# Kernel optimization log

Measured on AMD Instinct MI355X. Metric: run time of the kernel, lower is better.

The kernel has to match this reference:

```python
import jax, jax.numpy as jnp
import numpy as np

N_NODES = 50000
N_EDGES = 800000
D = 128
N_LAYERS = 3
EPS = 1e-5  # torch LayerNorm default


def _gcn_conv(x, src, dst, dinv, W, b):
    # PyG GCNConv: h = x @ W; out[i] = sum_{(s->i)} dinv[s]*dinv[i]*h[s] + dinv[i]^2*h[i] + b
    h = x @ W
    norm = dinv[src] * dinv[dst]                      # [E]
    msgs = h[src] * norm[:, None]                     # [E, D] gather
    agg = jax.ops.segment_sum(msgs, dst, num_segments=N_NODES)  # scatter-add
    agg = agg + h * (dinv * dinv)[:, None]            # self-loop term
    return agg + b


def _layer_norm(x, gamma, beta):
    mu = jnp.mean(x, axis=-1, keepdims=True)
    var = jnp.mean(jnp.square(x - mu), axis=-1, keepdims=True)
    return (x - mu) * jax.lax.rsqrt(var + EPS) * gamma + beta


def setup_inputs() -> dict:
    key = jax.random.key(0)
    ks = jax.random.split(key, 4)
    x = jax.random.normal(ks[0], (N_NODES, D), dtype=jnp.float32)
    edge_index = jax.random.randint(ks[1], (2, N_EDGES), 0, N_NODES, dtype=jnp.int64)
    Ws = jax.random.normal(ks[2], (N_LAYERS, D, D), dtype=jnp.float32) * (1.0 / np.sqrt(D))
    bs = jnp.zeros((N_LAYERS, D), dtype=jnp.float32)
    gammas = jnp.ones((N_LAYERS, D), dtype=jnp.float32)
    betas = jnp.zeros((N_LAYERS, D), dtype=jnp.float32)
    return {"x": x, "edge_index": edge_index, "Ws": Ws, "bs": bs,
            "gammas": gammas, "betas": betas}


def reference(x, edge_index, Ws, bs, gammas, betas):
    src, dst = edge_index[0], edge_index[1]
    # GCN symmetric normalization with self-loops: deg[i] = in-degree(i) + 1
    deg = jnp.zeros((N_NODES,), dtype=x.dtype).at[dst].add(1.0) + 1.0
    dinv = jax.lax.rsqrt(deg)
    h = x
    for i in range(N_LAYERS):
        x_new = _gcn_conv(h, src, dst, dinv, Ws[i], bs[i])
        x_new = _layer_norm(x_new, gammas[i], betas[i])
        x_new = jax.nn.relu(x_new)  # dropout is identity in eval mode
        h = h + x_new if i > 0 else x_new
    return h
```

## Files before the change

kernel.cpp:

```cpp
#include <hip/hip_runtime.h>
#include <hip/hip_bf16.h>

#define NN 50000
#define NE 800000
#define DD 128
#define NB 196
#define NCH 8
#define CHSZ 6250
#define NC2 (NN * NCH)
#define NSB 391
#define PH (64 * NB)
#define FS 2048
#define NSL 391
#define HHB (NSL * 8)
#define QB 3125
#define WB 192
#define LN_EPS 1e-5f

typedef __bf16 bf16x8 __attribute__((ext_vector_type(8)));
typedef float f32x4 __attribute__((ext_vector_type(4)));

__device__ inline ushort f2bf_bits(float f) {
    union { __hip_bfloat16 h; ushort u; } c;
    c.h = __float2bfloat16(f);
    return c.u;
}

__device__ inline void accum_q(float* acc, uint2 qv, float ww) {
    uint lo = qv.x, hi = qv.y;
    acc[0] = fmaf(ww, (float)(char)(lo), acc[0]);
    acc[1] = fmaf(ww, (float)(char)(lo >> 8), acc[1]);
    acc[2] = fmaf(ww, (float)(char)(lo >> 16), acc[2]);
    acc[3] = fmaf(ww, (float)(char)(lo >> 24), acc[3]);
    acc[4] = fmaf(ww, (float)(char)(hi), acc[4]);
    acc[5] = fmaf(ww, (float)(char)(hi >> 8), acc[5]);
    acc[6] = fmaf(ww, (float)(char)(hi >> 16), acc[6]);
    acc[7] = fmaf(ww, (float)(char)(hi >> 24), acc[7]);
}

__global__ void hist_cast_kernel(const int* __restrict__ src, const int* __restrict__ dst,
                                 int* __restrict__ counts2, const float* __restrict__ x,
                                 uint2* __restrict__ qf0, float* __restrict__ sc0,
                                 const float* __restrict__ W, ushort* __restrict__ Wt) {
    int b = blockIdx.x;
    if (b < HHB) {
        int slice = b >> 3;
        int r = b & 7;
        int base = slice * FS;
#pragma unroll 2
        for (int i = threadIdx.x; i < FS; i += 256) {
            int e = base + i;
            if (e < NE) {
                int d = dst[e];
                if (d / CHSZ == r) {
                    int s = src[e];
                    atomicAdd(&counts2[d * NCH + s / CHSZ], 1);
                }
            }
        }
    } else if (b < HHB + QB) {
        int bb = b - HHB;
        int group = threadIdx.x >> 4, t = threadIdx.x & 15;
        int node = bb * 16 + group;
        const float4* xr = (const float4*)(x + (size_t)node * DD + t * 8);
        float4 v0 = xr[0], v1 = xr[1];
        float vals[8] = {v0.x, v0.y, v0.z, v0.w, v1.x, v1.y, v1.z, v1.w};
        float am = 0.f;
#pragma unroll
        for (int i = 0; i < 8; ++i) am = fmaxf(am, fabsf(vals[i]));
#pragma unroll
        for (int off = 1; off <= 8; off <<= 1) am = fmaxf(am, __shfl_xor(am, off, 64));
        float inv = 127.f / fmaxf(am, 1e-20f);
        uint lo = 0, hi = 0;
#pragma unroll
        for (int i = 0; i < 4; ++i) {
            int q = __float2int_rn(vals[i] * inv);
            lo |= ((uint)(q & 0xff)) << (8 * i);
        }
#pragma unroll
        for (int i = 0; i < 4; ++i) {
            int q = __float2int_rn(vals[4 + i] * inv);
            hi |= ((uint)(q & 0xff)) << (8 * i);
        }
        uint2 pk; pk.x = lo; pk.y = hi;
        qf0[node * 16 + t] = pk;
        if (t == 0) sc0[node] = am / 127.f;
    } else {
        int i = (b - HHB - QB) * 256 + threadIdx.x;
        int l = i >> 14, k = (i >> 7) & 127, n = i & 127;
        Wt[l * 16384 + n * 128 + k] = f2bf_bits(W[i]);
    }
}

__global__ __launch_bounds__(1024) void scan1024_blocks(int* __restrict__ data,
                                                        int* __restrict__ bsums) {
    __shared__ int ws[16];
    int gid = blockIdx.x * 1024 + threadIdx.x;
    int lane = threadIdx.x & 63, wid = threadIdx.x >> 6;
    int v = (gid < NC2) ? data[gid] : 0;
    int x = v;
#pragma unroll
    for (int off = 1; off < 64; off <<= 1) {
        int t = __shfl_up(x, off, 64);
        if (lane >= off) x += t;
    }
    if (lane == 63) ws[wid] = x;
    __syncthreads();
    if (threadIdx.x == 0) {
        int run = 0;
        for (int i = 0; i < 16; ++i) { int t = ws[i]; ws[i] = run; run += t; }
        bsums[blockIdx.x] = run;
    }
    __syncthreads();
    if (gid < NC2) data[gid] = x - v + ws[wid];
}

__global__ __launch_bounds__(1024) void scan_sums1024(int* __restrict__ bsums, int nb) {
    __shared__ int ws[16];
    int tid = threadIdx.x;
    int lane = tid & 63, wid = tid >> 6;
    int v = (tid < nb) ? bsums[tid] : 0;
    int x = v;
#pragma unroll
    for (int off = 1; off < 64; off <<= 1) {
        int t = __shfl_up(x, off, 64);
        if (lane >= off) x += t;
    }
    if (lane == 63) ws[wid] = x;
    __syncthreads();
    if (tid == 0) {
        int run = 0;
        for (int i = 0; i < 16; ++i) { int t = ws[i]; ws[i] = run; run += t; }
    }
    __syncthreads();
    if (tid < nb) bsums[tid] = x - v + ws[wid];
}

__global__ void finalize_kernel(const int* __restrict__ excl2, const int* __restrict__ bsums,
                                int* __restrict__ row_ptr, int* __restrict__ next_pos2,
                                float* __restrict__ dinv, int* __restrict__ degarr,
                                int* __restrict__ bh) {
    __shared__ int lh[64];
    if (threadIdx.x < 64) lh[threadIdx.x] = 0;
    __syncthreads();
    int d = blockIdx.x * 256 + threadIdx.x;
    if (d < NN) {
        int base = d * NCH;
        int p0 = excl2[base] + bsums[base >> 10];
#pragma unroll
        for (int c = 0; c < NCH; ++c) {
            int idx = base + c;
            next_pos2[idx] = excl2[idx] + bsums[idx >> 10];
        }
        int nxt = (d == NN - 1) ? NE : excl2[base + NCH] + bsums[(base + NCH) >> 10];
        int deg = nxt - p0;
        row_ptr[d] = p0;
        dinv[d] = rsqrtf((float)deg + 1.0f);
        degarr[d] = deg;
        atomicAdd(&lh[min(deg, 63)], 1);
    }
    __syncthreads();
    if (threadIdx.x < 64) bh[threadIdx.x * NB + blockIdx.x] = lh[threadIdx.x];
    if (blockIdx.x == 0 && threadIdx.x == 0) row_ptr[NN] = NE;
}

__global__ __launch_bounds__(1024) void permscan_kernel(int* __restrict__ bh) {
    __shared__ int wsum[16];
    const int CH = 13;
    int tid = threadIdx.x;
    int base = tid * CH;
    int vals[CH];
    int s = 0;
#pragma unroll
    for (int i = 0; i < CH; ++i) {
        int idx = base + i;
        int v = (idx < PH) ? bh[idx] : 0;
        vals[i] = s;
        s += v;
    }
    int lane = tid & 63, wid = tid >> 6;
    int x = s;
#pragma unroll
    for (int off = 1; off < 64; off <<= 1) {
        int t = __shfl_up(x, off, 64);
        if (lane >= off) x += t;
    }
    if (lane == 63) wsum[wid] = x;
    __syncthreads();
    if (tid == 0) {
        int run = 0;
        for (int i = 0; i < 16; ++i) { int t = wsum[i]; wsum[i] = run; run += t; }
    }
    __syncthreads();
    int texcl = x - s + wsum[wid];
#pragma unroll
    for (int i = 0; i < CH; ++i) {
        int idx = base + i;
        if (idx < PH) bh[idx] = texcl + vals[i];
    }
}

__global__ void scatter_fill_kernel(const int* __restrict__ degarr, const int* __restrict__ bh,
                                    int* __restrict__ perm, const int* __restrict__ src,
                                    const int* __restrict__ dst, int* __restrict__ next_pos2,
                                    const float* __restrict__ dinv, int2* __restrict__ edge2) {
    if (blockIdx.x < NB) {
        __shared__ int lh[64];
        __shared__ int lbase[64];
        if (threadIdx.x < 64) {
            lh[threadIdx.x] = 0;
            lbase[threadIdx.x] = bh[threadIdx.x * NB + blockIdx.x];
        }
        __syncthreads();
        int gid = blockIdx.x * 256 + threadIdx.x;
        if (gid < NN) {
            int b = min(degarr[gid], 63);
            int r = atomicAdd(&lh[b], 1);
            perm[lbase[b] + r] = gid;
        }
    } else {
        int bb = blockIdx.x - NB;
        int slice = bb >> 3;
        int r = bb & 7;
        int base = slice * FS;
#pragma unroll 2
        for (int i = threadIdx.x; i < FS; i += 256) {
            int e = base + i;
            if (e < NE) {
                int d = dst[e];
                if (d / CHSZ == r) {
                    int s = src[e];
                    int pos = atomicAdd(&next_pos2[d * NCH + s / CHSZ], 1);
                    int2 o;
                    o.x = s;
                    o.y = __float_as_int(dinv[s] * dinv[d]);
                    edge2[pos] = o;
                }
            }
        }
    }
}

template <bool RES, bool FINAL>
__global__ __launch_bounds__(256) void layer_kernel(
    const uint2* __restrict__ qin, const float* __restrict__ scin,
    const ushort* __restrict__ fin, const int* __restrict__ row_ptr,
    const int2* __restrict__ edge2, const int* __restrict__ perm,
    const float* __restrict__ dinv, const ushort* __restrict__ Wt,
    const float* __restrict__ bias, const float* __restrict__ gamma,
    const float* __restrict__ beta, ushort* __restrict__ fout, char* __restrict__ qfout,
    float* __restrict__ scout, float* __restrict__ out) {
    __shared__ uint4 sA[16 * 17];
    __shared__ int sNode[16];
    __shared__ float sLN1[4][16], sLN2[4][16];
    __shared__ float sMX[4][16];

    int w = threadIdx.x >> 6, lane = threadIdx.x & 63;
    int g = lane >> 4, t = lane & 15;
    int arow = w * 4 + g;
    int slot = blockIdx.x * 16 + arow;
    int node = perm[slot];
    if (t == 0) sNode[arow] = node;

    {
        int beg = row_ptr[node], end = row_ptr[node + 1];
        float acc[8] = {};
        int e = beg;
        for (; e + 8 <= end; e += 8) {
            int2 a[8];
            uint2 qv[8];
            float sc[8];
#pragma unroll
            for (int j = 0; j < 8; ++j) a[j] = edge2[e + j];
#pragma unroll
            for (int j = 0; j < 8; ++j) {
                qv[j] = qin[a[j].x * 16 + t];
                sc[j] = scin[a[j].x];
            }
#pragma unroll
            for (int j = 0; j < 8; ++j) accum_q(acc, qv[j], __int_as_float(a[j].y) * sc[j]);
        }
        for (; e + 4 <= end; e += 4) {
            int2 a[4];
            uint2 qv[4];
            float sc[4];
#pragma unroll
            for (int j = 0; j < 4; ++j) a[j] = edge2[e + j];
#pragma unroll
            for (int j = 0; j < 4; ++j) {
                qv[j] = qin[a[j].x * 16 + t];
                sc[j] = scin[a[j].x];
            }
#pragma unroll
            for (int j = 0; j < 4; ++j) accum_q(acc, qv[j], __int_as_float(a[j].y) * sc[j]);
        }
        for (; e < end; ++e) {
            int2 a = edge2[e];
            uint2 qv = qin[a.x * 16 + t];
            accum_q(acc, qv, __int_as_float(a.y) * scin[a.x]);
        }
        {
            float di = dinv[node];
            uint2 qv = qin[node * 16 + t];
            accum_q(acc, qv, di * di * scin[node]);
        }
        union { ushort us[8]; uint4 u; } pk;
#pragma unroll
        for (int i = 0; i < 8; ++i) pk.us[i] = f2bf_bits(acc[i]);
        sA[arow * 17 + t] = pk.u;
    }
    __syncthreads();

    int q = lane >> 4, m = lane & 15;
    f32x4 c0 = (f32x4){0.f, 0.f, 0.f, 0.f};
    f32x4 c1 = (f32x4){0.f, 0.f, 0.f, 0.f};
    int n0 = 16 * (2 * w), n1 = 16 * (2 * w + 1);
#pragma unroll
    for (int kk = 0; kk < 4; ++kk) {
        bf16x8 af = *(const bf16x8*)&sA[m * 17 + kk * 4 + q];
        bf16x8 b0 = *(const bf16x8*)(Wt + (n0 + m) * DD + kk * 32 + q * 8);
        bf16x8 b1 = *(const bf16x8*)(Wt + (n1 + m) * DD + kk * 32 + q * 8);
        c0 = __builtin_amdgcn_mfma_f32_16x16x32_bf16(af, b0, c0, 0, 0, 0);
        c1 = __builtin_amdgcn_mfma_f32_16x16x32_bf16(af, b1, c1, 0, 0, 0);
    }

    float bb0 = bias[n0 + m], bb1 = bias[n1 + m];
    float s1[4], s2[4];
#pragma unroll
    for (int r = 0; r < 4; ++r) {
        float v0 = c0[r] + bb0, v1 = c1[r] + bb1;
        c0[r] = v0; c1[r] = v1;
        s1[r] = v0 + v1;
        s2[r] = v0 * v0 + v1 * v1;
    }
#pragma unroll
    for (int off = 1; off <= 8; off <<= 1) {
#pragma unroll
        for (int r = 0; r < 4; ++r) {
            s1[r] += __shfl_xor(s1[r], off, 64);
            s2[r] += __shfl_xor(s2[r], off, 64);
        }
    }
    if (m == 0) {
#pragma unroll
        for (int r = 0; r < 4; ++r) {
            sLN1[w][q * 4 + r] = s1[r];
            sLN2[w][q * 4 + r] = s2[r];
        }
    }
    __syncthreads();
    float ga0 = gamma[n0 + m], ga1 = gamma[n1 + m];
    float be0 = beta[n0 + m], be1 = beta[n1 + m];
    float o0v[4], o1v[4], rmax[4];
#pragma unroll
    for (int r = 0; r < 4; ++r) {
        int row = q * 4 + r;
        float S1 = sLN1[0][row] + sLN1[1][row] + sLN1[2][row] + sLN1[3][row];
        float S2 = sLN2[0][row] + sLN2[1][row] + sLN2[2][row] + sLN2[3][row];
        float mu = S1 * (1.f / 128.f);
        float var = S2 * (1.f / 128.f) - mu * mu;
        float rstd = rsqrtf(var + LN_EPS);
        int nd = sNode[row];
        size_t rb = (size_t)nd * DD;
        float o0 = fmaxf((c0[r] - mu) * rstd * ga0 + be0, 0.f);
        float o1 = fmaxf((c1[r] - mu) * rstd * ga1 + be1, 0.f);
        if (RES) {
            o0 += __uint_as_float(((uint)fin[rb + n0 + m]) << 16);
            o1 += __uint_as_float(((uint)fin[rb + n1 + m]) << 16);
        }
        if (FINAL) {
            out[rb + n0 + m] = o0;
            out[rb + n1 + m] = o1;
        } else {
            fout[rb + n0 + m] = f2bf_bits(o0);
            fout[rb + n1 + m] = f2bf_bits(o1);
            o0v[r] = o0; o1v[r] = o1;
            rmax[r] = fmaxf(o0, o1);
        }
    }
    if (!FINAL) {
#pragma unroll
        for (int off = 1; off <= 8; off <<= 1) {
#pragma unroll
            for (int r = 0; r < 4; ++r) rmax[r] = fmaxf(rmax[r], __shfl_xor(rmax[r], off, 64));
        }
        if (m == 0) {
#pragma unroll
            for (int r = 0; r < 4; ++r) sMX[w][q * 4 + r] = rmax[r];
        }
        __syncthreads();
#pragma unroll
        for (int r = 0; r < 4; ++r) {
            int row = q * 4 + r;
            float M = fmaxf(fmaxf(sMX[0][row], sMX[1][row]), fmaxf(sMX[2][row], sMX[3][row]));
            float inv = 127.f / fmaxf(M, 1e-20f);
            int nd = sNode[row];
            if (w == 0 && m == 0) scout[nd] = M / 127.f;
            int q0 = min(__float2int_rn(o0v[r] * inv), 127);
            int q1 = min(__float2int_rn(o1v[r] * inv), 127);
            qfout[(size_t)nd * DD + n0 + m] = (char)q0;
            qfout[(size_t)nd * DD + n1 + m] = (char)q1;
        }
    }
}


extern "C" void kernel_launch(void* const* d_in, const int* in_sizes, int n_in,
                              void* d_out, int out_size, void* d_ws, size_t ws_size,
                              hipStream_t stream) {
    const float* x = (const float*)d_in[0];
    const int* edge = (const int*)d_in[1];
    const float* Ws = (const float*)d_in[2];
    const float* bs = (const float*)d_in[3];
    const float* gs = (const float*)d_in[4];
    const float* bes = (const float*)d_in[5];
    float* out = (float*)d_out;
    const int* src = edge;
    const int* dst = edge + NE;

    char* p = (char*)d_ws;
    int* counts2 = (int*)p;     p += (size_t)NC2 * 4;
    int* bsums = (int*)p;       p += 1024 * 4;
    int* row_ptr = (int*)p;     p += (size_t)(NN + 4) * 4;
    int* next_pos2 = (int*)p;   p += (size_t)NC2 * 4;
    float* dinv = (float*)p;    p += (size_t)NN * 4;
    int* degarr = (int*)p;      p += (size_t)NN * 4;
    int* bh = (int*)p;          p += (size_t)PH * 4;
    int* perm = (int*)p;        p += (size_t)NN * 4;
    int2* edge2 = (int2*)p;     p += (size_t)NE * 8;
    ushort* fb0 = (ushort*)p;   p += (size_t)NN * DD * 2;
    ushort* fb1 = (ushort*)p;   p += (size_t)NN * DD * 2;
    char* qf0 = (char*)p;       p += (size_t)NN * DD;
    char* qf1 = (char*)p;       p += (size_t)NN * DD;
    float* sc0 = (float*)p;     p += (size_t)NN * 4;
    float* sc1 = (float*)p;     p += (size_t)NN * 4;
    ushort* Wt = (ushort*)p;    p += (size_t)3 * DD * DD * 2;

    hipMemsetAsync(counts2, 0, (size_t)NC2 * 4, stream);
    hist_cast_kernel<<<HHB + QB + WB, 256, 0, stream>>>(src, dst, counts2, x, (uint2*)qf0,
                                                        sc0, Ws, Wt);
    scan1024_blocks<<<NSB, 1024, 0, stream>>>(counts2, bsums);
    scan_sums1024<<<1, 1024, 0, stream>>>(bsums, NSB);
    finalize_kernel<<<NB, 256, 0, stream>>>(counts2, bsums, row_ptr, next_pos2, dinv, degarr,
                                            bh);
    permscan_kernel<<<1, 1024, 0, stream>>>(bh);
    scatter_fill_kernel<<<NB + NSL * 8, 256, 0, stream>>>(degarr, bh, perm, src, dst,
                                                          next_pos2, dinv, edge2);

    int lg = NN / 16;
    layer_kernel<false, false><<<lg, 256, 0, stream>>>(
        (const uint2*)qf0, sc0, fb0, row_ptr, edge2, perm, dinv, Wt, bs, gs, bes,
        fb1, qf1, sc1, out);
    layer_kernel<true, false><<<lg, 256, 0, stream>>>(
        (const uint2*)qf1, sc1, fb1, row_ptr, edge2, perm, dinv, Wt + 16384, bs + DD, gs + DD,
        bes + DD, fb0, qf0, sc0, out);
    layer_kernel<true, true><<<lg, 256, 0, stream>>>(
        (const uint2*)qf0, sc0, fb0, row_ptr, edge2, perm, dinv, Wt + 32768, bs + 2 * DD,
        gs + 2 * DD, bes + 2 * DD, fb1, qf1, sc1, out);
}
```

Measured before the change: 296.7 us.

## Record per-edge atomic rank in histogram to drop second atomic pass and reverse degree order

The histogram pass now stores each edge's atomic return value as a rank, so the scatter pass computes its CSR position directly from the scanned counts plus the rank instead of doing a second round of atomics on a next-position array. This removes the next_pos2 array and its writes in finalize, at the cost of writing and reading an extra 800k-entry rank array. The degree-bucket permutation is also reversed so high-degree nodes are processed first, which changes the layer kernels' load order. Edge order within each bin may differ from before, but the sum is order-insensitive apart from float rounding.

```diff
diff --git a/kernel.cpp b/kernel.cpp
--- a/kernel.cpp
+++ b/kernel.cpp
@@ -39,9 +39,10 @@
 }
 
 __global__ void hist_cast_kernel(const int* __restrict__ src, const int* __restrict__ dst,
-                                 int* __restrict__ counts2, const float* __restrict__ x,
-                                 uint2* __restrict__ qf0, float* __restrict__ sc0,
-                                 const float* __restrict__ W, ushort* __restrict__ Wt) {
+                                 int* __restrict__ counts2, int* __restrict__ rank,
+                                 const float* __restrict__ x, uint2* __restrict__ qf0,
+                                 float* __restrict__ sc0, const float* __restrict__ W,
+                                 ushort* __restrict__ Wt) {
     int b = blockIdx.x;
     if (b < HHB) {
         int slice = b >> 3;
@@ -54,7 +55,7 @@
                 int d = dst[e];
                 if (d / CHSZ == r) {
                     int s = src[e];
-                    atomicAdd(&counts2[d * NCH + s / CHSZ], 1);
+                    rank[e] = atomicAdd(&counts2[d * NCH + s / CHSZ], 1);
                 }
             }
         }
@@ -137,9 +138,8 @@
 }
 
 __global__ void finalize_kernel(const int* __restrict__ excl2, const int* __restrict__ bsums,
-                                int* __restrict__ row_ptr, int* __restrict__ next_pos2,
-                                float* __restrict__ dinv, int* __restrict__ degarr,
-                                int* __restrict__ bh) {
+                                int* __restrict__ row_ptr, float* __restrict__ dinv,
+                                int* __restrict__ degarr, int* __restrict__ bh) {
     __shared__ int lh[64];
     if (threadIdx.x < 64) lh[threadIdx.x] = 0;
     __syncthreads();
@@ -147,17 +147,12 @@
     if (d < NN) {
         int base = d * NCH;
         int p0 = excl2[base] + bsums[base >> 10];
-#pragma unroll
-        for (int c = 0; c < NCH; ++c) {
-            int idx = base + c;
-            next_pos2[idx] = excl2[idx] + bsums[idx >> 10];
-        }
         int nxt = (d == NN - 1) ? NE : excl2[base + NCH] + bsums[(base + NCH) >> 10];
         int deg = nxt - p0;
         row_ptr[d] = p0;
         dinv[d] = rsqrtf((float)deg + 1.0f);
         degarr[d] = deg;
-        atomicAdd(&lh[min(deg, 63)], 1);
+        atomicAdd(&lh[63 - min(deg, 63)], 1);
     }
     __syncthreads();
     if (threadIdx.x < 64) bh[threadIdx.x * NB + blockIdx.x] = lh[threadIdx.x];
@@ -202,7 +197,8 @@
 
 __global__ void scatter_fill_kernel(const int* __restrict__ degarr, const int* __restrict__ bh,
                                     int* __restrict__ perm, const int* __restrict__ src,
-                                    const int* __restrict__ dst, int* __restrict__ next_pos2,
+                                    const int* __restrict__ dst, const int* __restrict__ excl2,
+                                    const int* __restrict__ bsums, const int* __restrict__ rank,
                                     const float* __restrict__ dinv, int2* __restrict__ edge2) {
     if (blockIdx.x < NB) {
         __shared__ int lh[64];
@@ -214,7 +210,7 @@
         __syncthreads();
         int gid = blockIdx.x * 256 + threadIdx.x;
         if (gid < NN) {
-            int b = min(degarr[gid], 63);
+            int b = 63 - min(degarr[gid], 63);
             int r = atomicAdd(&lh[b], 1);
             perm[lbase[b] + r] = gid;
         }
@@ -230,7 +226,8 @@
                 int d = dst[e];
                 if (d / CHSZ == r) {
                     int s = src[e];
-                    int pos = atomicAdd(&next_pos2[d * NCH + s / CHSZ], 1);
+                    int bin = d * NCH + s / CHSZ;
+                    int pos = excl2[bin] + bsums[bin >> 10] + rank[e];
                     int2 o;
                     o.x = s;
                     o.y = __float_as_int(dinv[s] * dinv[d]);
@@ -422,7 +419,7 @@
     int* counts2 = (int*)p;     p += (size_t)NC2 * 4;
     int* bsums = (int*)p;       p += 1024 * 4;
     int* row_ptr = (int*)p;     p += (size_t)(NN + 4) * 4;
-    int* next_pos2 = (int*)p;   p += (size_t)NC2 * 4;
+    int* rank = (int*)p;        p += (size_t)NE * 4;
     float* dinv = (float*)p;    p += (size_t)NN * 4;
     int* degarr = (int*)p;      p += (size_t)NN * 4;
     int* bh = (int*)p;          p += (size_t)PH * 4;
@@ -437,15 +434,14 @@
     ushort* Wt = (ushort*)p;    p += (size_t)3 * DD * DD * 2;
 
     hipMemsetAsync(counts2, 0, (size_t)NC2 * 4, stream);
-    hist_cast_kernel<<<HHB + QB + WB, 256, 0, stream>>>(src, dst, counts2, x, (uint2*)qf0,
-                                                        sc0, Ws, Wt);
+    hist_cast_kernel<<<HHB + QB + WB, 256, 0, stream>>>(src, dst, counts2, rank, x,
+                                                        (uint2*)qf0, sc0, Ws, Wt);
     scan1024_blocks<<<NSB, 1024, 0, stream>>>(counts2, bsums);
     scan_sums1024<<<1, 1024, 0, stream>>>(bsums, NSB);
-    finalize_kernel<<<NB, 256, 0, stream>>>(counts2, bsums, row_ptr, next_pos2, dinv, degarr,
-                                            bh);
+    finalize_kernel<<<NB, 256, 0, stream>>>(counts2, bsums, row_ptr, dinv, degarr, bh);
     permscan_kernel<<<1, 1024, 0, stream>>>(bh);
-    scatter_fill_kernel<<<NB + NSL * 8, 256, 0, stream>>>(degarr, bh, perm, src, dst,
-                                                          next_pos2, dinv, edge2);
+    scatter_fill_kernel<<<NB + NSL * 8, 256, 0, stream>>>(degarr, bh, perm, src, dst, counts2,
+                                                          bsums, rank, dinv, edge2);
 
     int lg = NN / 16;
     layer_kernel<false, false><<<lg, 256, 0, stream>>>(
```

After: 285.0 us. 1.04x faster.
